# Kernel optimization log

Hardware: AMD Instinct MI355X
Metric: run time of the kernel (lower is better)

Reference implementation:

```python
import jax, jax.numpy as jnp
import numpy as np
from jax import lax

N, E, IN, OUT, H, OH = 2048, 16384, 128, 128, 4, 8
NEG_SLOPE = 0.2

def symlog(v):
    return jnp.sign(v) * jnp.log1p(jnp.abs(v))

def setup_inputs() -> dict:
    key = jax.random.key(0)
    ks = jax.random.split(key, 16)
    x = jax.random.normal(ks[0], (N, IN), dtype=jnp.float32)
    onehot = jax.random.uniform(ks[1], (N, N), dtype=jnp.float32)
    src = jax.random.randint(ks[2], (E,), 0, N, dtype=jnp.int32)
    # guarantee no self loops (original removes them before adding its own)
    off = jax.random.randint(ks[3], (E,), 1, N, dtype=jnp.int32)
    dst = (src + off) % N
    s = 0.05
    lin_w = jax.random.normal(ks[4], (H * OUT, IN + OH), dtype=jnp.float32) * s
    att_l = jax.random.normal(ks[5], (1, H, OUT), dtype=jnp.float32) * s
    att_r = jax.random.normal(ks[6], (1, H, OUT), dtype=jnp.float32) * s
    bias = jnp.zeros((H * OUT,), dtype=jnp.float32)
    conv1_w = jax.random.normal(ks[7], (8, 1, 3), dtype=jnp.float32) * s
    conv1_b = jnp.zeros((8,), dtype=jnp.float32)
    conv2_w = jax.random.normal(ks[8], (16, 8, 3), dtype=jnp.float32) * s
    conv2_b = jnp.zeros((16,), dtype=jnp.float32)
    fc_w = jax.random.normal(ks[9], (OH, 16), dtype=jnp.float32) * s
    fc_b = jnp.zeros((OH,), dtype=jnp.float32)
    return {"x": x, "onehot": onehot, "src": src, "dst": dst,
            "lin_w": lin_w, "att_l": att_l, "att_r": att_r, "bias": bias,
            "conv1_w": conv1_w, "conv1_b": conv1_b, "conv2_w": conv2_w,
            "conv2_b": conv2_b, "fc_w": fc_w, "fc_b": fc_b}

def _forward(x, onehot, src, dst, lin_w, att_l, att_r, bias,
             conv1_w, conv1_b, conv2_w, conv2_b, fc_w, fc_b):
    n = x.shape[0]
    # --- one-hot conv pipeline: sort -> symlog -> Conv1d x2 -> avgpool -> Linear ---
    prep = symlog(jnp.sort(onehot, axis=-1))[:, None, :]          # [N,1,N]
    dn = ('NCH', 'OIH', 'NCH')
    h = lax.conv_general_dilated(prep, conv1_w, (1,), [(1, 1)], dimension_numbers=dn)
    h = jax.nn.relu(h + conv1_b[None, :, None])                    # [N,8,N]
    h = lax.conv_general_dilated(h, conv2_w, (1,), [(1, 1)], dimension_numbers=dn)
    h = jax.nn.relu(h + conv2_b[None, :, None])                    # [N,16,N]
    pooled = h.mean(axis=-1)                                       # AdaptiveAvgPool1d(1) -> [N,16]
    oh_feat = pooled @ fc_w.T + fc_b                               # [N,OH]
    # --- linear + per-head attention logits ---
    xh = (jnp.concatenate([x, oh_feat], axis=-1) @ lin_w.T).reshape(n, H, OUT)
    sa = (xh * att_l).sum(-1)                                      # [N,H]
    ra = (xh * att_r).sum(-1)
    # --- add self loops (input edges contain none) ---
    loop = jnp.arange(n, dtype=src.dtype)
    s_i = jnp.concatenate([src, loop])
    d_i = jnp.concatenate([dst, loop])
    # --- message: LeakyReLU attention * one-hot dot attention ---
    alpha = jax.nn.leaky_relu(sa[s_i] + ra[d_i], NEG_SLOPE)        # [E',H]
    send_oh = onehot[s_i]                                          # [E',N]
    dotatt = 1.0 / ((symlog(send_oh) * symlog(onehot[d_i])).sum(axis=1) + 1.0)
    alpha = alpha * dotatt[:, None]
    # --- segment softmax over receiving node ---
    amax = jax.ops.segment_max(alpha, d_i, num_segments=n)
    ex = jnp.exp(alpha - amax[d_i])
    den = jax.ops.segment_sum(ex, d_i, num_segments=n)
    alpha = ex / (den[d_i] + 1e-16)
    # --- weighted aggregate (scatter-sum) ---
    agg_x = jax.ops.segment_sum(xh[s_i] * alpha[:, :, None], d_i, num_segments=n)
    agg_oh = jax.ops.segment_sum(send_oh, d_i, num_segments=n)
    new_x = agg_x.reshape(n, H * OUT) + bias                       # concat heads + bias
    new_onehot = onehot + agg_oh                                   # one_hot_incay='add'
    return new_x, new_onehot

def reference(x, onehot, src, dst, lin_w, att_l, att_r, bias,
              conv1_w, conv1_b, conv2_w, conv2_b, fc_w, fc_b):
    return _forward(x, onehot, src, dst, lin_w, att_l, att_r, bias,
                    conv1_w, conv1_b, conv2_w, conv2_b, fc_w, fc_b)
```

## Files before the change

kernel.cpp:

```cpp
#include <hip/hip_runtime.h>
#include <math.h>

#define NN   2048
#define NE   16384
#define NET  (NE + NN)
#define INF_ 128
#define OUTF 128
#define NH   4
#define OHF  8
#define NEG_SLOPE 0.2f
#define CAP  512

__device__ __forceinline__ float symlogf_(float v) {
    return copysignf(__logf(1.0f + fabsf(v)), v);
}

__global__ __launch_bounds__(256, 2) void k_sortconv(
    const float* __restrict__ onehot,
    const float* __restrict__ c1w, const float* __restrict__ c1b,
    const float* __restrict__ c2w, const float* __restrict__ c2b,
    const float* __restrict__ fcw, const float* __restrict__ fcb,
    float* __restrict__ slog, float* __restrict__ ohfeat) {
    __shared__ float soa[NN];
    __shared__ float bndL[4][2];
    __shared__ float bndR[4][2];
    __shared__ float red[64];
    __shared__ float pooled[16];
    const int t = threadIdx.x;
    const int r = blockIdx.x;
    const int b = t << 3;
    const int wave = t >> 6, lane = t & 63;
    const float* row  = onehot + (size_t)r * NN;
    float*       srow = slog   + (size_t)r * NN;

    float4 lo = ((const float4*)row)[t * 2];
    float4 hi = ((const float4*)row)[t * 2 + 1];
    float v[8] = {lo.x, lo.y, lo.z, lo.w, hi.x, hi.y, hi.z, hi.w};
    {
        float4 s0, s1;
        s0.x = symlogf_(v[0]); s0.y = symlogf_(v[1]);
        s0.z = symlogf_(v[2]); s0.w = symlogf_(v[3]);
        s1.x = symlogf_(v[4]); s1.y = symlogf_(v[5]);
        s1.z = symlogf_(v[6]); s1.w = symlogf_(v[7]);
        ((float4*)srow)[t * 2]     = s0;
        ((float4*)srow)[t * 2 + 1] = s1;
    }

    auto cx = [](float& x, float& y, bool up) {
        float mn = fminf(x, y), mx = fmaxf(x, y);
        x = up ? mn : mx;
        y = up ? mx : mn;
    };

    cx(v[0], v[1], true);  cx(v[2], v[3], false);
    cx(v[4], v[5], true);  cx(v[6], v[7], false);
    cx(v[0], v[2], true);  cx(v[1], v[3], true);
    cx(v[4], v[6], false); cx(v[5], v[7], false);
    cx(v[0], v[1], true);  cx(v[2], v[3], true);
    cx(v[4], v[5], false); cx(v[6], v[7], false);
    {
        const bool u8 = ((t & 1) == 0);
        cx(v[0], v[4], u8); cx(v[1], v[5], u8); cx(v[2], v[6], u8); cx(v[3], v[7], u8);
        cx(v[0], v[2], u8); cx(v[1], v[3], u8); cx(v[4], v[6], u8); cx(v[5], v[7], u8);
        cx(v[0], v[1], u8); cx(v[2], v[3], u8); cx(v[4], v[5], u8); cx(v[6], v[7], u8);
    }

    for (int k = 16; k <= NN; k <<= 1) {
        const bool up = ((b & k) == 0);
        for (int j = k >> 1; j >= 8; j >>= 1) {
            const int pj = j >> 3;
            const bool keepmin = (((t & pj) == 0) == up);
            if (pj <= 32) {
                #pragma unroll
                for (int e = 0; e < 8; e++) {
                    float p = __shfl_xor(v[e], pj, 64);
                    v[e] = keepmin ? fminf(v[e], p) : fmaxf(v[e], p);
                }
            } else {
                __syncthreads();
                #pragma unroll
                for (int e = 0; e < 8; e++) soa[e * 256 + t] = v[e];
                __syncthreads();
                const int pt = t ^ pj;
                #pragma unroll
                for (int e = 0; e < 8; e++) {
                    float p = soa[e * 256 + pt];
                    v[e] = keepmin ? fminf(v[e], p) : fmaxf(v[e], p);
                }
            }
        }
        cx(v[0], v[4], up); cx(v[1], v[5], up); cx(v[2], v[6], up); cx(v[3], v[7], up);
        cx(v[0], v[2], up); cx(v[1], v[3], up); cx(v[4], v[6], up); cx(v[5], v[7], up);
        cx(v[0], v[1], up); cx(v[2], v[3], up); cx(v[4], v[5], up); cx(v[6], v[7], up);
    }

    #pragma unroll
    for (int e = 0; e < 8; e++) v[e] = symlogf_(v[e]);

    __syncthreads();
    if (lane == 63) { bndL[wave][0] = v[6]; bndL[wave][1] = v[7]; }
    if (lane == 0)  { bndR[wave][0] = v[0]; bndR[wave][1] = v[1]; }
    __syncthreads();
    float vm2 = __shfl_up(v[6], 1, 64);
    float vm1 = __shfl_up(v[7], 1, 64);
    float vp8 = __shfl_down(v[0], 1, 64);
    float vp9 = __shfl_down(v[1], 1, 64);
    if (lane == 0) {
        vm2 = wave ? bndL[wave - 1][0] : 0.0f;
        vm1 = wave ? bndL[wave - 1][1] : 0.0f;
    }
    if (lane == 63) {
        vp8 = (wave < 3) ? bndR[wave + 1][0] : 0.0f;
        vp9 = (wave < 3) ? bndR[wave + 1][1] : 0.0f;
    }

    float vin[12];
    vin[0] = vm2; vin[1] = vm1;
    #pragma unroll
    for (int e = 0; e < 8; e++) vin[2 + e] = v[e];
    vin[10] = vp8; vin[11] = vp9;

    float h1c[10][8];
    {
        float w1[24], b1[8];
        #pragma unroll
        for (int q = 0; q < 24; q++) w1[q] = c1w[q];
        #pragma unroll
        for (int q = 0; q < 8; q++)  b1[q] = c1b[q];
        #pragma unroll
        for (int m = 0; m < 10; m++) {
            const float xm = vin[m], xc = vin[m + 1], xp = vin[m + 2];
            #pragma unroll
            for (int c = 0; c < 8; c++) {
                float a = fmaf(w1[c * 3 + 2], xp,
                          fmaf(w1[c * 3 + 1], xc,
                          fmaf(w1[c * 3 + 0], xm, b1[c])));
                h1c[m][c] = fmaxf(a, 0.0f);
            }
        }
        if (t == 0) {
            #pragma unroll
            for (int c = 0; c < 8; c++) h1c[0][c] = 0.0f;
        }
        if (t == 255) {
            #pragma unroll
            for (int c = 0; c < 8; c++) h1c[9][c] = 0.0f;
        }
    }

    float sums[16];
    #pragma unroll
    for (int ch = 0; ch < 16; ch++) {
        float wch[24];
        #pragma unroll
        for (int q = 0; q < 24; q++) wch[q] = c2w[ch * 24 + q];
        const float bb = c2b[ch];
        float acc = 0.0f;
        #pragma unroll
        for (int i = 0; i < 8; i++) {
            float a = bb;
            #pragma unroll
            for (int c = 0; c < 8; c++) {
                a = fmaf(wch[c * 3 + 0], h1c[i][c],     a);
                a = fmaf(wch[c * 3 + 1], h1c[i + 1][c], a);
                a = fmaf(wch[c * 3 + 2], h1c[i + 2][c], a);
            }
            acc += fmaxf(a, 0.0f);
        }
        sums[ch] = acc;
    }

    #pragma unroll
    for (int c = 0; c < 16; c++)
        for (int o = 32; o; o >>= 1) sums[c] += __shfl_down(sums[c], o);
    if (lane == 0)
        #pragma unroll
        for (int c = 0; c < 16; c++) red[wave * 16 + c] = sums[c];
    __syncthreads();
    if (t < 16)
        pooled[t] = (red[t] + red[16 + t] + red[32 + t] + red[48 + t]) * (1.0f / NN);
    __syncthreads();
    if (t < OHF) {
        float a = fcb[t];
        #pragma unroll
        for (int c = 0; c < 16; c++) a = fmaf(fcw[t * 16 + c], pooled[c], a);
        ohfeat[r * OHF + t] = a;
    }
}

__global__ __launch_bounds__(256) void k_xh(
    const float* __restrict__ x, const float* __restrict__ ohf,
    const float* __restrict__ lin_w, const float* __restrict__ att_l,
    const float* __restrict__ att_r, float* __restrict__ xh,
    float* __restrict__ sa, float* __restrict__ ra) {
    const int n0 = blockIdx.x * 4;
    __shared__ float xin[4][136];
    __shared__ float part[4][16];
    const int tid = threadIdx.x;
    const int wave = tid >> 6, lane = tid & 63;
    for (int i = tid; i < 4 * 136; i += 256) {
        int nn = i / 136, k = i - nn * 136;
        xin[nn][k] = (k < INF_) ? x[(size_t)(n0+nn)*INF_ + k]
                                : ohf[(n0+nn)*OHF + (k - INF_)];
    }
    __syncthreads();
    float accl[2][4], accr[2][4];
    #pragma unroll
    for (int g = 0; g < 2; g++)
        #pragma unroll
        for (int n = 0; n < 4; n++) { accl[g][n] = 0.0f; accr[g][n] = 0.0f; }

    #pragma unroll
    for (int g = 0; g < 2; g++) {
        const int o = tid + g * 256;
        const float4* wr4 = (const float4*)(lin_w + (size_t)o * 136);
        float a0 = 0, a1 = 0, a2 = 0, a3 = 0;
        for (int kk = 0; kk < 34; kk++) {
            float4 w = wr4[kk];
            int k = kk * 4;
            a0 += w.x*xin[0][k] + w.y*xin[0][k+1] + w.z*xin[0][k+2] + w.w*xin[0][k+3];
            a1 += w.x*xin[1][k] + w.y*xin[1][k+1] + w.z*xin[1][k+2] + w.w*xin[1][k+3];
            a2 += w.x*xin[2][k] + w.y*xin[2][k+1] + w.z*xin[2][k+2] + w.w*xin[2][k+3];
            a3 += w.x*xin[3][k] + w.y*xin[3][k+1] + w.z*xin[3][k+2] + w.w*xin[3][k+3];
        }
        xh[(size_t)(n0+0)*512 + o] = a0;
        xh[(size_t)(n0+1)*512 + o] = a1;
        xh[(size_t)(n0+2)*512 + o] = a2;
        xh[(size_t)(n0+3)*512 + o] = a3;
        const float al = att_l[o], ar = att_r[o];
        accl[g][0] = fmaf(a0, al, accl[g][0]); accr[g][0] = fmaf(a0, ar, accr[g][0]);
        accl[g][1] = fmaf(a1, al, accl[g][1]); accr[g][1] = fmaf(a1, ar, accr[g][1]);
        accl[g][2] = fmaf(a2, al, accl[g][2]); accr[g][2] = fmaf(a2, ar, accr[g][2]);
        accl[g][3] = fmaf(a3, al, accl[g][3]); accr[g][3] = fmaf(a3, ar, accr[g][3]);
    }
    #pragma unroll
    for (int g = 0; g < 2; g++)
        #pragma unroll
        for (int n = 0; n < 4; n++)
            for (int o = 32; o; o >>= 1) {
                accl[g][n] += __shfl_down(accl[g][n], o);
                accr[g][n] += __shfl_down(accr[g][n], o);
            }
    if (lane == 0) {
        #pragma unroll
        for (int g = 0; g < 2; g++)
            #pragma unroll
            for (int n = 0; n < 4; n++) {
                part[wave][n * 4 + g * 2 + 0] = accl[g][n];
                part[wave][n * 4 + g * 2 + 1] = accr[g][n];
            }
    }
    __syncthreads();
    if (tid < 32) {
        const int n = tid >> 3, rem = tid & 7, h = rem >> 1, lr = rem & 1;
        const int g = h >> 1, wp = (h & 1) * 2;
        const float val = part[wp][n * 4 + g * 2 + lr] + part[wp + 1][n * 4 + g * 2 + lr];
        if (lr == 0) sa[(n0 + n) * 4 + h] = val;
        else         ra[(n0 + n) * 4 + h] = val;
    }
}

__global__ void k_count(const int* __restrict__ dst, int* __restrict__ deg) {
    int e = blockIdx.x * 256 + threadIdx.x;
    if (e < NET) {
        int d = (e < NE) ? dst[e] : (e - NE);
        atomicAdd(&deg[d], 1);
    }
}

__global__ __launch_bounds__(256) void k_scan(
    const int* __restrict__ deg, int* __restrict__ csr_off,
    int* __restrict__ csr_pos) {
    __shared__ int wsum[4];
    const int t = threadIdx.x, wave = t >> 6, lane = t & 63;
    int loc[8], s = 0;
    #pragma unroll
    for (int k = 0; k < 8; k++) { loc[k] = deg[t*8 + k]; s += loc[k]; }
    int x = s;
    for (int o = 1; o < 64; o <<= 1) {
        int u = __shfl_up(x, o, 64);
        if (lane >= o) x += u;
    }
    if (lane == 63) wsum[wave] = x;
    __syncthreads();
    int off = 0;
    #pragma unroll
    for (int w = 0; w < 4; w++) if (w < wave) off += wsum[w];
    int base = off + x - s;
    #pragma unroll
    for (int k = 0; k < 8; k++) {
        csr_off[t*8 + k] = base;
        csr_pos[t*8 + k] = base;
        base += loc[k];
    }
    if (t == 255) csr_off[NN] = off + x;
}

__global__ void k_fill(const int* __restrict__ dst, int* __restrict__ csr_pos,
                       int* __restrict__ csr_e) {
    int e = blockIdx.x * 256 + threadIdx.x;
    if (e < NET) {
        int d = (e < NE) ? dst[e] : (e - NE);
        int pos = atomicAdd(&csr_pos[d], 1);
        csr_e[pos] = e;
    }
}

__global__ __launch_bounds__(256) void k_datt(
    const int* __restrict__ src, const int* __restrict__ dst,
    const float* __restrict__ slog, float* __restrict__ datt) {
    const int e = blockIdx.x * 4 + (threadIdx.x >> 6);
    const int lane = threadIdx.x & 63;
    int s, d;
    if (e < NE) { s = src[e]; d = dst[e]; } else { s = d = e - NE; }
    const float4* A = (const float4*)(slog + (size_t)s * NN);
    const float4* B = (const float4*)(slog + (size_t)d * NN);
    float p = 0.0f;
    #pragma unroll
    for (int i = 0; i < 8; i++) {
        float4 a = A[lane + 64 * i];
        float4 b = B[lane + 64 * i];
        p = fmaf(a.x, b.x, p); p = fmaf(a.y, b.y, p);
        p = fmaf(a.z, b.z, p); p = fmaf(a.w, b.w, p);
    }
    #pragma unroll
    for (int o = 32; o; o >>= 1) p += __shfl_down(p, o);
    if (lane == 0) datt[e] = 1.0f / (p + 1.0f);
}

__global__ __launch_bounds__(256) void k_agg(
    const int* __restrict__ src, const int* __restrict__ csr_off,
    const int* __restrict__ csr_e, const float* __restrict__ datt,
    const float* __restrict__ sa, const float* __restrict__ ra,
    const float* __restrict__ xh, const float* __restrict__ onehot,
    const float* __restrict__ bias, float* __restrict__ out_x,
    float* __restrict__ out_oh) {
    const int d = blockIdx.x;
    const int begin = csr_off[d];
    int deg = csr_off[d + 1] - begin;
    if (deg > CAP) deg = CAP;
    __shared__ float wls[CAP * 4];
    __shared__ int   sls[CAP];
    const int tid = threadIdx.x;
    const float4 rav = *(const float4*)(ra + d * 4);
    for (int t = tid; t < deg; t += 256) {
        int e = csr_e[begin + t];
        int s = (e < NE) ? src[e] : (e - NE);
        sls[t] = s;
        float4 sav = *(const float4*)(sa + s * 4);
        float dt = datt[e];
        float a0 = sav.x + rav.x; a0 = (a0 >= 0.0f ? a0 : NEG_SLOPE * a0) * dt;
        float a1 = sav.y + rav.y; a1 = (a1 >= 0.0f ? a1 : NEG_SLOPE * a1) * dt;
        float a2 = sav.z + rav.z; a2 = (a2 >= 0.0f ? a2 : NEG_SLOPE * a2) * dt;
        float a3 = sav.w + rav.w; a3 = (a3 >= 0.0f ? a3 : NEG_SLOPE * a3) * dt;
        wls[t*4 + 0] = a0; wls[t*4 + 1] = a1;
        wls[t*4 + 2] = a2; wls[t*4 + 3] = a3;
    }
    __syncthreads();
    const int wave = tid >> 6, lane = tid & 63;
    {
        float m = -3.4e38f;
        for (int t = lane; t < deg; t += 64) m = fmaxf(m, wls[t*4 + wave]);
        for (int o = 32; o; o >>= 1) m = fmaxf(m, __shfl_down(m, o));
        m = __shfl(m, 0);
        float s = 0.0f;
        for (int t = lane; t < deg; t += 64) {
            float ex = expf(wls[t*4 + wave] - m);
            wls[t*4 + wave] = ex;
            s += ex;
        }
        for (int o = 32; o; o >>= 1) s += __shfl_down(s, o);
        s = __shfl(s, 0);
        float inv = 1.0f / (s + 1e-16f);
        for (int t = lane; t < deg; t += 64) wls[t*4 + wave] *= inv;
    }
    __syncthreads();
    const int h = tid >> 6;
    float2 accx; accx.x = 0.0f; accx.y = 0.0f;
    const float4* own = (const float4*)(onehot + (size_t)d * NN);
    float4 A = own[tid], B = own[tid + 256];
    const float2* xh2 = (const float2*)xh;
    const float4* oh4 = (const float4*)onehot;
    for (int t = 0; t < deg; t++) {
        const float w = wls[t*4 + h];
        const int s = sls[t];
        float2 xv = xh2[(size_t)s * 256 + tid];
        accx.x = fmaf(w, xv.x, accx.x);
        accx.y = fmaf(w, xv.y, accx.y);
        float4 u  = oh4[(size_t)s * 512 + tid];
        float4 vv = oh4[(size_t)s * 512 + 256 + tid];
        A.x += u.x;  A.y += u.y;  A.z += u.z;  A.w += u.w;
        B.x += vv.x; B.y += vv.y; B.z += vv.z; B.w += vv.w;
    }
    float2 bv = ((const float2*)bias)[tid];
    float2 outv; outv.x = accx.x + bv.x; outv.y = accx.y + bv.y;
    ((float2*)out_x)[(size_t)d * 256 + tid] = outv;
    float4* o4 = (float4*)(out_oh + (size_t)d * NN);
    o4[tid] = A; o4[tid + 256] = B;
}

extern "C" void kernel_launch(void* const* d_in, const int* in_sizes, int n_in,
                              void* d_out, int out_size, void* d_ws, size_t ws_size,
                              hipStream_t stream) {
    const float* x      = (const float*)d_in[0];
    const float* onehot = (const float*)d_in[1];
    const int*   src    = (const int*)d_in[2];
    const int*   dst    = (const int*)d_in[3];
    const float* lin_w  = (const float*)d_in[4];
    const float* att_l  = (const float*)d_in[5];
    const float* att_r  = (const float*)d_in[6];
    const float* bias   = (const float*)d_in[7];
    const float* c1w    = (const float*)d_in[8];
    const float* c1b    = (const float*)d_in[9];
    const float* c2w    = (const float*)d_in[10];
    const float* c2b    = (const float*)d_in[11];
    const float* fcw    = (const float*)d_in[12];
    const float* fcb    = (const float*)d_in[13];

    float* out_x  = (float*)d_out;
    float* out_oh = out_x + (size_t)NN * (NH * OUTF);

    float* ws    = (float*)d_ws;
    float* slog  = ws;
    float* xh    = slog + (size_t)NN * NN;
    float* ohf   = xh   + (size_t)NN * 512;
    float* sa    = ohf  + (size_t)NN * OHF;
    float* ra    = sa   + (size_t)NN * NH;
    float* datt  = ra   + (size_t)NN * NH;
    int* deg     = (int*)(datt + (size_t)NET);
    int* csr_off = deg + NN;
    int* csr_pos = csr_off + NN + 1;
    int* csr_e   = csr_pos + NN;

    hipMemsetAsync(deg, 0, NN * sizeof(int), stream);
    k_sortconv<<<NN, 256, 0, stream>>>(onehot, c1w, c1b, c2w, c2b, fcw, fcb, slog, ohf);
    k_count<<<(NET + 255) / 256, 256, 0, stream>>>(dst, deg);
    k_scan<<<1, 256, 0, stream>>>(deg, csr_off, csr_pos);
    k_fill<<<(NET + 255) / 256, 256, 0, stream>>>(dst, csr_pos, csr_e);
    k_xh<<<NN / 4, 256, 0, stream>>>(x, ohf, lin_w, att_l, att_r, xh, sa, ra);
    k_datt<<<NET / 4, 256, 0, stream>>>(src, dst, slog, datt);
    k_agg<<<NN, 256, 0, stream>>>(src, csr_off, csr_e, datt, sa, ra, xh, onehot,
                                  bias, out_x, out_oh);
}
```

Baseline: 292.1 us.

## Fuse self-loop dot attention into sortconv and merge CSR build into one kernel

The self-loop dot-attention term (sum of squared symlog values) is now computed inside the sort/conv kernel from data already in registers, so k_datt only handles the real edges. The count/scan/fill CSR build is merged into a single 1024-thread block that uses shared-memory atomics, which removes a memset and two launches. The sortconv launch bounds are raised to 4 blocks per CU, which may cause register spills in that heavy kernel. CSR construction now runs on one CU, serialising that small amount of work.

```diff
diff --git a/kernel.cpp b/kernel.cpp
--- a/kernel.cpp
+++ b/kernel.cpp
@@ -15,16 +15,18 @@
     return copysignf(__logf(1.0f + fabsf(v)), v);
 }
 
-__global__ __launch_bounds__(256, 2) void k_sortconv(
+__global__ __launch_bounds__(256, 4) void k_sortconv(
     const float* __restrict__ onehot,
     const float* __restrict__ c1w, const float* __restrict__ c1b,
     const float* __restrict__ c2w, const float* __restrict__ c2b,
     const float* __restrict__ fcw, const float* __restrict__ fcb,
-    float* __restrict__ slog, float* __restrict__ ohfeat) {
+    float* __restrict__ slog, float* __restrict__ ohfeat,
+    float* __restrict__ datt) {
     __shared__ float soa[NN];
     __shared__ float bndL[4][2];
     __shared__ float bndR[4][2];
     __shared__ float red[64];
+    __shared__ float red2[4];
     __shared__ float pooled[16];
     const int t = threadIdx.x;
     const int r = blockIdx.x;
@@ -97,6 +99,10 @@
     #pragma unroll
     for (int e = 0; e < 8; e++) v[e] = symlogf_(v[e]);
 
+    float ssq = 0.0f;
+    #pragma unroll
+    for (int e = 0; e < 8; e++) ssq = fmaf(v[e], v[e], ssq);
+
     __syncthreads();
     if (lane == 63) { bndL[wave][0] = v[6]; bndL[wave][1] = v[7]; }
     if (lane == 0)  { bndR[wave][0] = v[0]; bndR[wave][1] = v[1]; }
@@ -173,12 +179,18 @@
     #pragma unroll
     for (int c = 0; c < 16; c++)
         for (int o = 32; o; o >>= 1) sums[c] += __shfl_down(sums[c], o);
-    if (lane == 0)
+    #pragma unroll
+    for (int o = 32; o; o >>= 1) ssq += __shfl_down(ssq, o);
+    if (lane == 0) {
         #pragma unroll
         for (int c = 0; c < 16; c++) red[wave * 16 + c] = sums[c];
+        red2[wave] = ssq;
+    }
     __syncthreads();
     if (t < 16)
         pooled[t] = (red[t] + red[16 + t] + red[32 + t] + red[48 + t]) * (1.0f / NN);
+    if (t == 16)
+        datt[NE + r] = 1.0f / (red2[0] + red2[1] + red2[2] + red2[3] + 1.0f);
     __syncthreads();
     if (t < OHF) {
         float a = fcb[t];
@@ -260,49 +272,44 @@
     }
 }
 
-__global__ void k_count(const int* __restrict__ dst, int* __restrict__ deg) {
-    int e = blockIdx.x * 256 + threadIdx.x;
-    if (e < NET) {
+__global__ __launch_bounds__(1024) void k_csr(
+    const int* __restrict__ dst, int* __restrict__ csr_off,
+    int* __restrict__ csr_e) {
+    __shared__ int cnt[NN];
+    __shared__ int wtot[16];
+    const int t = threadIdx.x;
+    const int wave = t >> 6, lane = t & 63;
+    for (int i = t; i < NN; i += 1024) cnt[i] = 0;
+    __syncthreads();
+    for (int e = t; e < NET; e += 1024) {
         int d = (e < NE) ? dst[e] : (e - NE);
-        atomicAdd(&deg[d], 1);
-    }
-}
-
-__global__ __launch_bounds__(256) void k_scan(
-    const int* __restrict__ deg, int* __restrict__ csr_off,
-    int* __restrict__ csr_pos) {
-    __shared__ int wsum[4];
-    const int t = threadIdx.x, wave = t >> 6, lane = t & 63;
-    int loc[8], s = 0;
-    #pragma unroll
-    for (int k = 0; k < 8; k++) { loc[k] = deg[t*8 + k]; s += loc[k]; }
+        atomicAdd(&cnt[d], 1);
+    }
+    __syncthreads();
+    int c0 = cnt[2 * t], c1 = cnt[2 * t + 1];
+    int s = c0 + c1;
     int x = s;
     for (int o = 1; o < 64; o <<= 1) {
         int u = __shfl_up(x, o, 64);
         if (lane >= o) x += u;
     }
-    if (lane == 63) wsum[wave] = x;
+    if (lane == 63) wtot[wave] = x;
     __syncthreads();
     int off = 0;
     #pragma unroll
-    for (int w = 0; w < 4; w++) if (w < wave) off += wsum[w];
-    int base = off + x - s;
-    #pragma unroll
-    for (int k = 0; k < 8; k++) {
-        csr_off[t*8 + k] = base;
-        csr_pos[t*8 + k] = base;
-        base += loc[k];
-    }
-    if (t == 255) csr_off[NN] = off + x;
-}
-
-__global__ void k_fill(const int* __restrict__ dst, int* __restrict__ csr_pos,
-                       int* __restrict__ csr_e) {
-    int e = blockIdx.x * 256 + threadIdx.x;
-    if (e < NET) {
+    for (int w = 0; w < 16; w++) if (w < wave) off += wtot[w];
+    const int base = off + x - s;
+    csr_off[2 * t]     = base;
+    csr_off[2 * t + 1] = base + c0;
+    if (t == 1023) csr_off[NN] = off + x;
+    __syncthreads();
+    cnt[2 * t]     = base;
+    cnt[2 * t + 1] = base + c0;
+    __syncthreads();
+    for (int e = t; e < NET; e += 1024) {
         int d = (e < NE) ? dst[e] : (e - NE);
-        int pos = atomicAdd(&csr_pos[d], 1);
-        csr_e[pos] = e;
+        int p = atomicAdd(&cnt[d], 1);
+        csr_e[p] = e;
     }
 }
 
@@ -311,8 +318,7 @@
     const float* __restrict__ slog, float* __restrict__ datt) {
     const int e = blockIdx.x * 4 + (threadIdx.x >> 6);
     const int lane = threadIdx.x & 63;
-    int s, d;
-    if (e < NE) { s = src[e]; d = dst[e]; } else { s = d = e - NE; }
+    const int s = src[e], d = dst[e];
     const float4* A = (const float4*)(slog + (size_t)s * NN);
     const float4* B = (const float4*)(slog + (size_t)d * NN);
     float p = 0.0f;
@@ -427,18 +433,14 @@
     float* sa    = ohf  + (size_t)NN * OHF;
     float* ra    = sa   + (size_t)NN * NH;
     float* datt  = ra   + (size_t)NN * NH;
-    int* deg     = (int*)(datt + (size_t)NET);
-    int* csr_off = deg + NN;
-    int* csr_pos = csr_off + NN + 1;
-    int* csr_e   = csr_pos + NN;
-
-    hipMemsetAsync(deg, 0, NN * sizeof(int), stream);
-    k_sortconv<<<NN, 256, 0, stream>>>(onehot, c1w, c1b, c2w, c2b, fcw, fcb, slog, ohf);
-    k_count<<<(NET + 255) / 256, 256, 0, stream>>>(dst, deg);
-    k_scan<<<1, 256, 0, stream>>>(deg, csr_off, csr_pos);
-    k_fill<<<(NET + 255) / 256, 256, 0, stream>>>(dst, csr_pos, csr_e);
+    int* csr_off = (int*)(datt + (size_t)NET);
+    int* csr_e   = csr_off + NN + 1;
+
+    k_sortconv<<<NN, 256, 0, stream>>>(onehot, c1w, c1b, c2w, c2b, fcw, fcb,
+                                       slog, ohf, datt);
+    k_csr<<<1, 1024, 0, stream>>>(dst, csr_off, csr_e);
     k_xh<<<NN / 4, 256, 0, stream>>>(x, ohf, lin_w, att_l, att_r, xh, sa, ra);
-    k_datt<<<NET / 4, 256, 0, stream>>>(src, dst, slog, datt);
+    k_datt<<<NE / 4, 256, 0, stream>>>(src, dst, slog, datt);
     k_agg<<<NN, 256, 0, stream>>>(src, csr_off, csr_e, datt, sa, ra, xh, onehot,
                                   bias, out_x, out_oh);
 }
```

New measurement: 286.2 us. 1.02x faster.
